# Kernel optimization log

Measured on AMD Instinct MI355X. Metric: run time of the kernel, lower is better.

Reference implementation:

```python
import jax, jax.numpy as jnp
import numpy as np

N_NODES = 500000
N_EDGES = 8000000
IN_DIM = 128
H1, H2, OUT = 32, 16, 2


def gcn_conv(x, W, b, src, dst, n):
    # PyG GCNConv: linear transform, add self-loops, symmetric norm, scatter-add, +bias
    x = x @ W                                   # [N, out]
    loop = jnp.arange(n, dtype=src.dtype)
    s = jnp.concatenate([src, loop])            # [E+N]
    d = jnp.concatenate([dst, loop])            # [E+N]
    deg = jax.ops.segment_sum(jnp.ones_like(d, dtype=x.dtype), d, num_segments=n)
    dinv = jnp.where(deg > 0, jax.lax.rsqrt(deg), 0.0)
    norm = dinv[s] * dinv[d]                    # [E+N]
    msg = x[s] * norm[:, None]                  # [E+N, out] gather
    out = jax.ops.segment_sum(msg, d, num_segments=n)  # scatter-add
    return out + b


def setup_inputs() -> dict:
    key = jax.random.key(0)
    ks = jax.random.split(key, 8)
    x = jax.random.normal(ks[0], (N_NODES, IN_DIM), dtype=jnp.float32)
    edge_index = jax.random.randint(ks[1], (2, N_EDGES), 0, N_NODES, dtype=jnp.int64)
    def glorot(k, fan_in, fan_out):
        lim = float(np.sqrt(6.0 / (fan_in + fan_out)))
        return jax.random.uniform(k, (fan_in, fan_out), jnp.float32, -lim, lim)
    return {
        "x": x,
        "edge_index": edge_index,
        "W1": glorot(ks[2], IN_DIM, H1),
        "b1": jnp.zeros((H1,), jnp.float32),
        "W2": glorot(ks[3], H1, H2),
        "b2": jnp.zeros((H2,), jnp.float32),
        "Wfc": glorot(ks[4], H2, OUT),
        "bfc": jnp.zeros((OUT,), jnp.float32),
    }


def reference(x, edge_index, W1, b1, W2, b2, Wfc, bfc):
    src, dst = edge_index[0], edge_index[1]
    h = jax.nn.relu(gcn_conv(x, W1, b1, src, dst, x.shape[0]))
    h = jax.nn.relu(gcn_conv(h, W2, b2, src, dst, x.shape[0]))
    logits = h @ Wfc + bfc
    return jax.nn.log_softmax(logits, axis=1)
```

## Files before the change

### kernel.cpp

```cpp
#include <hip/hip_runtime.h>

#define N_NODES 500000
#define N_EDGES 8000000
#define IN_DIM 128
#define H1 32
#define H2 16
#define NFINE 1954
#define NCOARSE 62
#define CAPA 200
#define CAPB 340

static __device__ __forceinline__ float bf2f(unsigned short u) {
    return __uint_as_float(((unsigned int)u) << 16);
}
static __device__ __forceinline__ unsigned short f2bf(float f) {
    unsigned int u = __float_as_uint(f);
    unsigned int r = (u + 0x7fffu + ((u >> 16) & 1u)) >> 16;
    return (unsigned short)r;
}
static __device__ __forceinline__ unsigned pack2bf(float a, float b) {
    return (unsigned)f2bf(a) | ((unsigned)f2bf(b) << 16);
}
static __device__ __forceinline__ float ldf(const void* p, int i, bool isf32) {
    return isf32 ? ((const float*)p)[i] : bf2f(((const unsigned short*)p)[i]);
}

__global__ __launch_bounds__(64) void k_sniff(const unsigned int* __restrict__ x,
                                              int* __restrict__ flag) {
    int bad = 0;
    for (int i = threadIdx.x; i < 1024; i += 64) {
        float v = __uint_as_float((x[i] & 0xffffu) << 16);
        if (!(fabsf(v) < 1e6f)) bad = 1;
    }
    unsigned long long m = __ballot(bad);
    if (threadIdx.x == 0) *flag = (m != 0ull) ? 1 : 0;
}

__global__ __launch_bounds__(256) void k_bhist(const int* __restrict__ dst,
                                               int* __restrict__ fhist) {
    __shared__ int h[2048];
    int tid = threadIdx.x;
    for (int i = tid; i < 2048; i += 256) h[i] = 0;
    __syncthreads();
    int i = blockIdx.x * 256 + tid;
    int stride = gridDim.x * 256;
    for (int e = i; e < N_EDGES; e += stride) {
        unsigned d = (unsigned)dst[e];
        if (d < N_NODES) atomicAdd(&h[d >> 8], 1);
    }
    __syncthreads();
    for (int i2 = tid; i2 < 2048; i2 += 256)
        if (h[i2]) atomicAdd(&fhist[i2], h[i2]);
}

__global__ __launch_bounds__(256) void k_scanf(const int* __restrict__ fhist,
                                               int* __restrict__ fbase,
                                               int* __restrict__ bcur,
                                               int* __restrict__ acur) {
    __shared__ int tmp[256];
    __shared__ int s_run;
    int tid = threadIdx.x;
    if (tid == 0) s_run = 0;
    __syncthreads();
    for (int base = 0; base < 2048; base += 256) {
        int i = base + tid;
        int v = (i < NFINE) ? fhist[i] : 0;
        int val = v;
        tmp[tid] = val;
        __syncthreads();
        for (int o = 1; o < 256; o <<= 1) {
            int t = (tid >= o) ? tmp[tid - o] : 0;
            __syncthreads();
            val += t;
            tmp[tid] = val;
            __syncthreads();
        }
        int run = s_run;
        if (i < NFINE) {
            int ex = run + val - v;
            fbase[i] = ex;
            bcur[i] = ex;
            if ((i & 31) == 0) acur[i >> 5] = ex;
        }
        __syncthreads();
        if (tid == 255) s_run = run + val;
        __syncthreads();
    }
    if (tid == 0) fbase[NFINE] = s_run;
}

__global__ __launch_bounds__(256) void k_scatA(const int* __restrict__ src,
                                               const int* __restrict__ dst,
                                               int* __restrict__ acur,
                                               unsigned* __restrict__ ebufA) {
    __shared__ unsigned stage[NCOARSE * CAPA];
    __shared__ int lcnt[NCOARSE], nn[NCOARSE], soff[NCOARSE], sbase[NCOARSE];
    __shared__ int stot;
    int tid = threadIdx.x;
    int cb = blockIdx.x * 8192;
    if (tid < NCOARSE) lcnt[tid] = 0;
    __syncthreads();
    for (int i = 0; i < 32; ++i) {
        int e = cb + (i << 8) + tid;
        if (e < N_EDGES) {
            unsigned d = (unsigned)dst[e], s = (unsigned)src[e];
            if (d < N_NODES) {
                unsigned b = d >> 13;
                unsigned p = ((d & 8191u) << 19) | s;
                int pos = atomicAdd(&lcnt[b], 1);
                if (pos < CAPA) stage[b * CAPA + pos] = p;
                else { int slot = atomicAdd(&acur[b], 1); ebufA[slot] = p; }
            }
        }
    }
    __syncthreads();
    if (tid < NCOARSE) nn[tid] = min(lcnt[tid], CAPA);
    __syncthreads();
    if (tid == 0) {
        int r = 0;
        for (int b = 0; b < NCOARSE; ++b) { soff[b] = r; r += nn[b]; }
        stot = r;
    }
    __syncthreads();
    if (tid < NCOARSE && nn[tid] > 0) sbase[tid] = atomicAdd(&acur[tid], nn[tid]);
    __syncthreads();
    for (int i = tid; i < stot; i += 256) {
        int lo = 0, hi = NCOARSE - 1;
        while (lo < hi) { int mid = (lo + hi + 1) >> 1; if (soff[mid] <= i) lo = mid; else hi = mid - 1; }
        int r = i - soff[lo];
        ebufA[sbase[lo] + r] = stage[lo * CAPA + r];
    }
}

__global__ __launch_bounds__(256) void k_scatB(const unsigned* __restrict__ ebufA,
                                               const int* __restrict__ fbase,
                                               int* __restrict__ bcur,
                                               unsigned* __restrict__ ebufB) {
    __shared__ unsigned stage[32 * CAPB];
    __shared__ int lcnt[32], nn[32], soff[32], sbase[32];
    __shared__ int stot;
    int tid = threadIdx.x;
    int a = blockIdx.x >> 3, sub = blockIdx.x & 7;
    int f0 = a * 32;
    int lb = min(32, NFINE - f0);
    int abase = fbase[f0];
    int aend = fbase[min(f0 + 32, NFINE)];
    for (int cb = abase + sub * 8192; cb < aend; cb += 8 * 8192) {
        if (tid < 32) lcnt[tid] = 0;
        __syncthreads();
        for (int i = 0; i < 32; ++i) {
            int e = cb + (i << 8) + tid;
            if (e < aend) {
                unsigned p = ebufA[e];
                unsigned dl13 = p >> 19;
                unsigned s = p & 0x7FFFFu;
                unsigned j = dl13 >> 8;
                unsigned q = ((dl13 & 255u) << 19) | s;
                int pos = atomicAdd(&lcnt[j], 1);
                if (pos < CAPB) stage[j * CAPB + pos] = q;
                else { int slot = atomicAdd(&bcur[f0 + j], 1); ebufB[slot] = q; }
            }
        }
        __syncthreads();
        if (tid < 32) nn[tid] = (tid < lb) ? min(lcnt[tid], CAPB) : 0;
        __syncthreads();
        if (tid == 0) {
            int r = 0;
            for (int b = 0; b < 32; ++b) { soff[b] = r; r += nn[b]; }
            stot = r;
        }
        __syncthreads();
        if (tid < 32 && nn[tid] > 0) sbase[tid] = atomicAdd(&bcur[f0 + tid], nn[tid]);
        __syncthreads();
        for (int i = tid; i < stot; i += 256) {
            int lo = 0, hi = 31;
            while (lo < hi) { int mid = (lo + hi + 1) >> 1; if (soff[mid] <= i) lo = mid; else hi = mid - 1; }
            int r = i - soff[lo];
            ebufB[sbase[lo] + r] = stage[lo * CAPB + r];
        }
        __syncthreads();
    }
}

__global__ __launch_bounds__(256) void k_csr(const unsigned* __restrict__ ebufB,
                                             const int* __restrict__ fbase,
                                             int* __restrict__ csr,
                                             int* __restrict__ off,
                                             float* __restrict__ dinv) {
    __shared__ int cnt[256], ctmp[256], ccur[256];
    int tid = threadIdx.x;
    int b = blockIdx.x;
    int base = fbase[b];
    int n = fbase[b + 1] - base;
    cnt[tid] = 0;
    __syncthreads();
    for (int i = tid; i < n; i += 256) {
        unsigned dl = ebufB[base + i] >> 19;
        atomicAdd(&cnt[dl], 1);
    }
    __syncthreads();
    int v = cnt[tid];
    int val = v;
    ctmp[tid] = val;
    __syncthreads();
    for (int o = 1; o < 256; o <<= 1) {
        int t = (tid >= o) ? ctmp[tid - o] : 0;
        __syncthreads();
        val += t;
        ctmp[tid] = val;
        __syncthreads();
    }
    int excl = val - v;
    off[b * 256 + tid] = base + excl;
    ccur[tid] = excl;
    dinv[b * 256 + tid] = rsqrtf((float)v + 1.0f);
    __syncthreads();
    for (int i = tid; i < n; i += 256) {
        unsigned p = ebufB[base + i];
        unsigned dl = p >> 19;
        int slot = atomicAdd(&ccur[dl], 1);
        csr[base + slot] = (int)(p & 0x7FFFFu);
    }
}

__global__ __launch_bounds__(256) void k_gemm1(const void* __restrict__ x,
                                               const void* __restrict__ w1,
                                               const float* __restrict__ dinv,
                                               unsigned* __restrict__ y1b,
                                               const int* __restrict__ flag) {
    __shared__ float wlds[IN_DIM * H1];
    const bool isf32 = (*flag != 0);
    for (int i = threadIdx.x; i < IN_DIM * H1; i += 256) wlds[i] = ldf(w1, i, isf32);
    __syncthreads();
    int node = blockIdx.x * 256 + threadIdx.x;
    if (node >= N_NODES) return;
    float acc[H1];
#pragma unroll
    for (int j = 0; j < H1; ++j) acc[j] = 0.f;
    if (isf32) {
        const float4* xr = reinterpret_cast<const float4*>((const float*)x + (size_t)node * IN_DIM);
#pragma unroll
        for (int kk = 0; kk < IN_DIM / 4; ++kk) {
            float4 v = xr[kk];
            float xe[4] = {v.x, v.y, v.z, v.w};
#pragma unroll
            for (int p = 0; p < 4; ++p) {
                const float* wr = &wlds[(kk * 4 + p) * H1];
#pragma unroll
                for (int j = 0; j < H1; ++j) acc[j] += xe[p] * wr[j];
            }
        }
    } else {
        const uint4* xr = reinterpret_cast<const uint4*>((const unsigned short*)x + (size_t)node * IN_DIM);
#pragma unroll
        for (int kk = 0; kk < IN_DIM / 8; ++kk) {
            uint4 xv = xr[kk];
            unsigned uu[4] = {xv.x, xv.y, xv.z, xv.w};
#pragma unroll
            for (int p = 0; p < 4; ++p) {
                float xlo = __uint_as_float(uu[p] << 16);
                float xhi = __uint_as_float(uu[p] & 0xffff0000u);
                const float* w0 = &wlds[(kk * 8 + p * 2) * H1];
                const float* w1r = w0 + H1;
#pragma unroll
                for (int j = 0; j < H1; ++j) acc[j] += xlo * w0[j];
#pragma unroll
                for (int j = 0; j < H1; ++j) acc[j] += xhi * w1r[j];
            }
        }
    }
    float s = dinv[node];
    unsigned o[16];
#pragma unroll
    for (int q = 0; q < 16; ++q) o[q] = pack2bf(acc[2*q] * s, acc[2*q+1] * s);
    uint4* op = reinterpret_cast<uint4*>(y1b + (size_t)node * 16);
#pragma unroll
    for (int r = 0; r < 4; ++r) op[r] = make_uint4(o[4*r], o[4*r+1], o[4*r+2], o[4*r+3]);
}

__global__ __launch_bounds__(256) void k_pull1(const int* __restrict__ off,
                                               const int* __restrict__ csr,
                                               const unsigned* __restrict__ y1b,
                                               const float* __restrict__ dinv,
                                               const void* __restrict__ b1,
                                               const void* __restrict__ w2,
                                               unsigned* __restrict__ y2b,
                                               const int* __restrict__ flag) {
    __shared__ float w2l[H1 * H2];
    __shared__ float b1l[H1];
    __shared__ float hbuf[512];
    const bool isf32 = (*flag != 0);
    int tid = threadIdx.x;
    for (int i = tid; i < H1 * H2; i += 256) w2l[i] = ldf(w2, i, isf32);
    if (tid < H1) b1l[tid] = ldf(b1, tid, isf32);
    __syncthreads();

    const int r = tid & 15;
    const int node = blockIdx.x * 16 + (tid >> 4);

    float a0 = 0.f, a1 = 0.f;
    const int beg = off[node], end = off[node + 1];
    int j = beg;
    for (; j + 4 <= end; j += 4) {
        int s0 = csr[j], s1 = csr[j + 1], s2 = csr[j + 2], s3 = csr[j + 3];
        unsigned u0 = y1b[(size_t)s0 * 16 + r];
        unsigned u1 = y1b[(size_t)s1 * 16 + r];
        unsigned u2 = y1b[(size_t)s2 * 16 + r];
        unsigned u3 = y1b[(size_t)s3 * 16 + r];
        a0 += __uint_as_float(u0 << 16) + __uint_as_float(u1 << 16)
            + __uint_as_float(u2 << 16) + __uint_as_float(u3 << 16);
        a1 += __uint_as_float(u0 & 0xffff0000u) + __uint_as_float(u1 & 0xffff0000u)
            + __uint_as_float(u2 & 0xffff0000u) + __uint_as_float(u3 & 0xffff0000u);
    }
    for (; j < end; ++j) {
        unsigned u = y1b[(size_t)csr[j] * 16 + r];
        a0 += __uint_as_float(u << 16);
        a1 += __uint_as_float(u & 0xffff0000u);
    }
    float sc = dinv[node];
    unsigned su = y1b[(size_t)node * 16 + r];
    a0 += __uint_as_float(su << 16);
    a1 += __uint_as_float(su & 0xffff0000u);
    float h0 = sc * a0 + b1l[2 * r];
    float h1 = sc * a1 + b1l[2 * r + 1];
    h0 = h0 > 0.f ? h0 : 0.f;
    h1 = h1 > 0.f ? h1 : 0.f;
    hbuf[tid * 2] = h0;
    hbuf[tid * 2 + 1] = h1;
    const float* hr = &hbuf[(tid & ~15) * 2];
    float a2 = 0.f;
#pragma unroll
    for (int k = 0; k < H1; ++k) a2 += hr[k] * w2l[k * H2 + r];
    a2 *= sc;
    int gwb = (tid & 63) & ~15;
    float v0 = __shfl(a2, (gwb + 2 * r) & 63, 64);
    float v1 = __shfl(a2, (gwb + 2 * r + 1) & 63, 64);
    if (r < 8) y2b[(size_t)node * 8 + r] = pack2bf(v0, v1);
}

__global__ __launch_bounds__(256) void k_pull2(const int* __restrict__ off,
                                               const int* __restrict__ csr,
                                               const unsigned* __restrict__ y2b,
                                               const float* __restrict__ dinv,
                                               const void* __restrict__ b2,
                                               const void* __restrict__ wfc,
                                               const void* __restrict__ bfc,
                                               void* __restrict__ out,
                                               const int* __restrict__ flag) {
    __shared__ float wl[H2 * 2];
    __shared__ float b2l[H2];
    __shared__ float bfl[2];
    const bool isf32 = (*flag != 0);
    int tid = threadIdx.x;
    if (tid < H2 * 2) wl[tid] = ldf(wfc, tid, isf32);
    if (tid < H2) b2l[tid] = ldf(b2, tid, isf32);
    if (tid < 2) bfl[tid] = ldf(bfc, tid, isf32);
    __syncthreads();

    const int r = tid & 7;
    const int node = blockIdx.x * 32 + (tid >> 3);

    float a0 = 0.f, a1 = 0.f;
    const int beg = off[node], end = off[node + 1];
    int j = beg;
    for (; j + 4 <= end; j += 4) {
        int s0 = csr[j], s1 = csr[j + 1], s2 = csr[j + 2], s3 = csr[j + 3];
        unsigned u0 = y2b[(size_t)s0 * 8 + r];
        unsigned u1 = y2b[(size_t)s1 * 8 + r];
        unsigned u2 = y2b[(size_t)s2 * 8 + r];
        unsigned u3 = y2b[(size_t)s3 * 8 + r];
        a0 += __uint_as_float(u0 << 16) + __uint_as_float(u1 << 16)
            + __uint_as_float(u2 << 16) + __uint_as_float(u3 << 16);
        a1 += __uint_as_float(u0 & 0xffff0000u) + __uint_as_float(u1 & 0xffff0000u)
            + __uint_as_float(u2 & 0xffff0000u) + __uint_as_float(u3 & 0xffff0000u);
    }
    for (; j < end; ++j) {
        unsigned u = y2b[(size_t)csr[j] * 8 + r];
        a0 += __uint_as_float(u << 16);
        a1 += __uint_as_float(u & 0xffff0000u);
    }
    float sc = dinv[node];
    unsigned su = y2b[(size_t)node * 8 + r];
    a0 += __uint_as_float(su << 16);
    a1 += __uint_as_float(su & 0xffff0000u);
    float h0 = sc * a0 + b2l[2 * r];
    float h1 = sc * a1 + b2l[2 * r + 1];
    h0 = h0 > 0.f ? h0 : 0.f;
    h1 = h1 > 0.f ? h1 : 0.f;
    float l0 = h0 * wl[4 * r]     + h1 * wl[4 * r + 2];
    float l1 = h0 * wl[4 * r + 1] + h1 * wl[4 * r + 3];
#pragma unroll
    for (int o = 4; o >= 1; o >>= 1) {
        l0 += __shfl_xor(l0, o, 8);
        l1 += __shfl_xor(l1, o, 8);
    }
    if (r == 0) {
        l0 += bfl[0];
        l1 += bfl[1];
        float mx = fmaxf(l0, l1);
        float lse = mx + logf(__expf(l0 - mx) + __expf(l1 - mx));
        if (isf32) {
            reinterpret_cast<float2*>(out)[node] = make_float2(l0 - lse, l1 - lse);
        } else {
            reinterpret_cast<unsigned*>(out)[node] =
                (unsigned)f2bf(l0 - lse) | ((unsigned)f2bf(l1 - lse) << 16);
        }
    }
}

extern "C" void kernel_launch(void* const* d_in, const int* in_sizes, int n_in,
                              void* d_out, int out_size, void* d_ws, size_t ws_size,
                              hipStream_t stream) {
    const void* x   = d_in[0];
    const int*  ei  = (const int*)d_in[1];
    const void* w1  = d_in[2];
    const void* b1  = d_in[3];
    const void* w2  = d_in[4];
    const void* b2  = d_in[5];
    const void* wfc = d_in[6];
    const void* bfc = d_in[7];
    const int* src = ei;
    const int* dst = ei + N_EDGES;

    float*    ws    = (float*)d_ws;
    int*      flag  = (int*)ws;
    float*    dinv  = ws + 64;
    int*      fhist = (int*)(ws + 500288);
    int*      fbase = (int*)(ws + 502336);
    int*      acur  = (int*)(ws + 504384);
    int*      bcur  = (int*)(ws + 504448);
    int*      off   = (int*)(ws + 506496);
    unsigned* ebufA = (unsigned*)(ws + 1006784);
    int*      csr   = (int*)(ws + 1006784);
    unsigned* ebufB = (unsigned*)(ws + 9006784);
    unsigned* y1b   = (unsigned*)(ws + 17006784);
    unsigned* y2b   = (unsigned*)(ws + 25010368);

    k_sniff<<<1, 64, 0, stream>>>((const unsigned int*)x, flag);
    hipMemsetAsync(fhist, 0, 2048 * sizeof(int), stream);
    k_bhist<<<256, 256, 0, stream>>>(dst, fhist);
    k_scanf<<<1, 256, 0, stream>>>(fhist, fbase, bcur, acur);
    k_scatA<<<977, 256, 0, stream>>>(src, dst, acur, ebufA);
    k_scatB<<<NCOARSE * 8, 256, 0, stream>>>(ebufA, fbase, bcur, ebufB);
    k_csr<<<NFINE, 256, 0, stream>>>(ebufB, fbase, csr, off, dinv);
    k_gemm1<<<NFINE, 256, 0, stream>>>(x, w1, dinv, y1b, flag);
    k_pull1<<<31250, 256, 0, stream>>>(off, csr, y1b, dinv, b1, w2, y2b, flag);
    k_pull2<<<15625, 256, 0, stream>>>(off, csr, y2b, dinv, b2, wfc, bfc, d_out, flag);
}
```

Baseline: 1.039 ms.

## Use 16-byte vector gathers with fewer threads per node in pull kernels

Both aggregation kernels now give each thread 8 bf16 features and load them with one uint4 per neighbor, instead of one 32-bit word per lane. This means 4 threads per node in layer 1 and 2 per node in layer 2, with a clamped, masked 4-way unrolled edge loop and no scalar tail. The layer-2 transform reads a padded shared buffer per node, and the final reduction shrinks to a single shuffle. The aim is fewer memory instructions and more nodes per block. The cost is more registers and more per-thread serial work on high-degree nodes.

```diff
diff --git a/kernel.cpp b/kernel.cpp
--- a/kernel.cpp
+++ b/kernel.cpp
@@ -23,6 +23,17 @@
 }
 static __device__ __forceinline__ float ldf(const void* p, int i, bool isf32) {
     return isf32 ? ((const float*)p)[i] : bf2f(((const unsigned short*)p)[i]);
+}
+static __device__ __forceinline__ uint4 zsel(uint4 u, int v) {
+    return v ? u : make_uint4(0u, 0u, 0u, 0u);
+}
+static __device__ __forceinline__ void acc8(float a[8], uint4 u) {
+    unsigned w[4] = {u.x, u.y, u.z, u.w};
+#pragma unroll
+    for (int p = 0; p < 4; ++p) {
+        a[2 * p]     += __uint_as_float(w[p] << 16);
+        a[2 * p + 1] += __uint_as_float(w[p] & 0xffff0000u);
+    }
 }
 
 __global__ __launch_bounds__(64) void k_sniff(const unsigned int* __restrict__ x,
@@ -288,54 +299,60 @@
                                                const int* __restrict__ flag) {
     __shared__ float w2l[H1 * H2];
     __shared__ float b1l[H1];
-    __shared__ float hbuf[512];
+    __shared__ float hbuf[64 * 33];
     const bool isf32 = (*flag != 0);
     int tid = threadIdx.x;
     for (int i = tid; i < H1 * H2; i += 256) w2l[i] = ldf(w2, i, isf32);
     if (tid < H1) b1l[tid] = ldf(b1, tid, isf32);
     __syncthreads();
 
-    const int r = tid & 15;
-    const int node = blockIdx.x * 16 + (tid >> 4);
-
-    float a0 = 0.f, a1 = 0.f;
+    const int r = tid & 3;
+    const int g = tid >> 2;
+    const int node = blockIdx.x * 64 + g;
+    if (node >= N_NODES) return;
+
+    float a[8];
+#pragma unroll
+    for (int p = 0; p < 8; ++p) a[p] = 0.f;
+
     const int beg = off[node], end = off[node + 1];
-    int j = beg;
-    for (; j + 4 <= end; j += 4) {
-        int s0 = csr[j], s1 = csr[j + 1], s2 = csr[j + 2], s3 = csr[j + 3];
-        unsigned u0 = y1b[(size_t)s0 * 16 + r];
-        unsigned u1 = y1b[(size_t)s1 * 16 + r];
-        unsigned u2 = y1b[(size_t)s2 * 16 + r];
-        unsigned u3 = y1b[(size_t)s3 * 16 + r];
-        a0 += __uint_as_float(u0 << 16) + __uint_as_float(u1 << 16)
-            + __uint_as_float(u2 << 16) + __uint_as_float(u3 << 16);
-        a1 += __uint_as_float(u0 & 0xffff0000u) + __uint_as_float(u1 & 0xffff0000u)
-            + __uint_as_float(u2 & 0xffff0000u) + __uint_as_float(u3 & 0xffff0000u);
-    }
-    for (; j < end; ++j) {
-        unsigned u = y1b[(size_t)csr[j] * 16 + r];
-        a0 += __uint_as_float(u << 16);
-        a1 += __uint_as_float(u & 0xffff0000u);
-    }
-    float sc = dinv[node];
-    unsigned su = y1b[(size_t)node * 16 + r];
-    a0 += __uint_as_float(su << 16);
-    a1 += __uint_as_float(su & 0xffff0000u);
-    float h0 = sc * a0 + b1l[2 * r];
-    float h1 = sc * a1 + b1l[2 * r + 1];
-    h0 = h0 > 0.f ? h0 : 0.f;
-    h1 = h1 > 0.f ? h1 : 0.f;
-    hbuf[tid * 2] = h0;
-    hbuf[tid * 2 + 1] = h1;
-    const float* hr = &hbuf[(tid & ~15) * 2];
-    float a2 = 0.f;
-#pragma unroll
-    for (int k = 0; k < H1; ++k) a2 += hr[k] * w2l[k * H2 + r];
-    a2 *= sc;
-    int gwb = (tid & 63) & ~15;
-    float v0 = __shfl(a2, (gwb + 2 * r) & 63, 64);
-    float v1 = __shfl(a2, (gwb + 2 * r + 1) & 63, 64);
-    if (r < 8) y2b[(size_t)node * 8 + r] = pack2bf(v0, v1);
+    const unsigned* yb = y1b + 4 * r;
+    for (int j = beg; j < end; j += 4) {
+        const int e1 = end - 1;
+        int i1 = min(j + 1, e1), i2 = min(j + 2, e1), i3 = min(j + 3, e1);
+        int s0 = csr[j], s1 = csr[i1], s2 = csr[i2], s3 = csr[i3];
+        uint4 u0 = *reinterpret_cast<const uint4*>(yb + (size_t)s0 * 16);
+        uint4 u1 = *reinterpret_cast<const uint4*>(yb + (size_t)s1 * 16);
+        uint4 u2 = *reinterpret_cast<const uint4*>(yb + (size_t)s2 * 16);
+        uint4 u3 = *reinterpret_cast<const uint4*>(yb + (size_t)s3 * 16);
+        u1 = zsel(u1, j + 1 < end);
+        u2 = zsel(u2, j + 2 < end);
+        u3 = zsel(u3, j + 3 < end);
+        acc8(a, u0); acc8(a, u1); acc8(a, u2); acc8(a, u3);
+    }
+    uint4 su = *reinterpret_cast<const uint4*>(yb + (size_t)node * 16);
+    acc8(a, su);
+
+    const float sc = dinv[node];
+    float* hb = &hbuf[g * 33];
+#pragma unroll
+    for (int p = 0; p < 8; ++p) {
+        float h = sc * a[p] + b1l[8 * r + p];
+        hb[8 * r + p] = h > 0.f ? h : 0.f;
+    }
+    float z[4];
+#pragma unroll
+    for (int c = 0; c < 4; ++c) z[c] = 0.f;
+#pragma unroll
+    for (int k = 0; k < H1; ++k) {
+        float hv = hb[k];
+#pragma unroll
+        for (int c = 0; c < 4; ++c) z[c] += hv * w2l[k * H2 + 4 * r + c];
+    }
+    uint2 o;
+    o.x = pack2bf(sc * z[0], sc * z[1]);
+    o.y = pack2bf(sc * z[2], sc * z[3]);
+    *reinterpret_cast<uint2*>(y2b + (size_t)node * 8 + 2 * r) = o;
 }
 
 __global__ __launch_bounds__(256) void k_pull2(const int* __restrict__ off,
@@ -357,43 +374,43 @@
     if (tid < 2) bfl[tid] = ldf(bfc, tid, isf32);
     __syncthreads();
 
-    const int r = tid & 7;
-    const int node = blockIdx.x * 32 + (tid >> 3);
-
-    float a0 = 0.f, a1 = 0.f;
+    const int r = tid & 1;
+    const int node = blockIdx.x * 128 + (tid >> 1);
+    if (node >= N_NODES) return;
+
+    float a[8];
+#pragma unroll
+    for (int p = 0; p < 8; ++p) a[p] = 0.f;
+
     const int beg = off[node], end = off[node + 1];
-    int j = beg;
-    for (; j + 4 <= end; j += 4) {
-        int s0 = csr[j], s1 = csr[j + 1], s2 = csr[j + 2], s3 = csr[j + 3];
-        unsigned u0 = y2b[(size_t)s0 * 8 + r];
-        unsigned u1 = y2b[(size_t)s1 * 8 + r];
-        unsigned u2 = y2b[(size_t)s2 * 8 + r];
-        unsigned u3 = y2b[(size_t)s3 * 8 + r];
-        a0 += __uint_as_float(u0 << 16) + __uint_as_float(u1 << 16)
-            + __uint_as_float(u2 << 16) + __uint_as_float(u3 << 16);
-        a1 += __uint_as_float(u0 & 0xffff0000u) + __uint_as_float(u1 & 0xffff0000u)
-            + __uint_as_float(u2 & 0xffff0000u) + __uint_as_float(u3 & 0xffff0000u);
-    }
-    for (; j < end; ++j) {
-        unsigned u = y2b[(size_t)csr[j] * 8 + r];
-        a0 += __uint_as_float(u << 16);
-        a1 += __uint_as_float(u & 0xffff0000u);
-    }
-    float sc = dinv[node];
-    unsigned su = y2b[(size_t)node * 8 + r];
-    a0 += __uint_as_float(su << 16);
-    a1 += __uint_as_float(su & 0xffff0000u);
-    float h0 = sc * a0 + b2l[2 * r];
-    float h1 = sc * a1 + b2l[2 * r + 1];
-    h0 = h0 > 0.f ? h0 : 0.f;
-    h1 = h1 > 0.f ? h1 : 0.f;
-    float l0 = h0 * wl[4 * r]     + h1 * wl[4 * r + 2];
-    float l1 = h0 * wl[4 * r + 1] + h1 * wl[4 * r + 3];
-#pragma unroll
-    for (int o = 4; o >= 1; o >>= 1) {
-        l0 += __shfl_xor(l0, o, 8);
-        l1 += __shfl_xor(l1, o, 8);
-    }
+    const unsigned* yb = y2b + 4 * r;
+    for (int j = beg; j < end; j += 4) {
+        const int e1 = end - 1;
+        int i1 = min(j + 1, e1), i2 = min(j + 2, e1), i3 = min(j + 3, e1);
+        int s0 = csr[j], s1 = csr[i1], s2 = csr[i2], s3 = csr[i3];
+        uint4 u0 = *reinterpret_cast<const uint4*>(yb + (size_t)s0 * 8);
+        uint4 u1 = *reinterpret_cast<const uint4*>(yb + (size_t)s1 * 8);
+        uint4 u2 = *reinterpret_cast<const uint4*>(yb + (size_t)s2 * 8);
+        uint4 u3 = *reinterpret_cast<const uint4*>(yb + (size_t)s3 * 8);
+        u1 = zsel(u1, j + 1 < end);
+        u2 = zsel(u2, j + 2 < end);
+        u3 = zsel(u3, j + 3 < end);
+        acc8(a, u0); acc8(a, u1); acc8(a, u2); acc8(a, u3);
+    }
+    uint4 su = *reinterpret_cast<const uint4*>(yb + (size_t)node * 8);
+    acc8(a, su);
+
+    const float sc = dinv[node];
+    float l0 = 0.f, l1 = 0.f;
+#pragma unroll
+    for (int p = 0; p < 8; ++p) {
+        float h = sc * a[p] + b2l[8 * r + p];
+        h = h > 0.f ? h : 0.f;
+        l0 += h * wl[(8 * r + p) * 2];
+        l1 += h * wl[(8 * r + p) * 2 + 1];
+    }
+    l0 += __shfl_xor(l0, 1, 64);
+    l1 += __shfl_xor(l1, 1, 64);
     if (r == 0) {
         l0 += bfl[0];
         l1 += bfl[1];
@@ -444,6 +461,6 @@
     k_scatB<<<NCOARSE * 8, 256, 0, stream>>>(ebufA, fbase, bcur, ebufB);
     k_csr<<<NFINE, 256, 0, stream>>>(ebufB, fbase, csr, off, dinv);
     k_gemm1<<<NFINE, 256, 0, stream>>>(x, w1, dinv, y1b, flag);
-    k_pull1<<<31250, 256, 0, stream>>>(off, csr, y1b, dinv, b1, w2, y2b, flag);
-    k_pull2<<<15625, 256, 0, stream>>>(off, csr, y2b, dinv, b2, wfc, bfc, d_out, flag);
-}
+    k_pull1<<<(N_NODES + 63) / 64, 256, 0, stream>>>(off, csr, y1b, dinv, b1, w2, y2b, flag);
+    k_pull2<<<(N_NODES + 127) / 128, 256, 0, stream>>>(off, csr, y2b, dinv, b2, wfc, bfc, d_out, flag);
+}
```

Result: no change. 1.020 ms (-1.8%).
